# Performance work log

Hardware: AMD Instinct MI355X
Metric: run time of the kernel (lower is better)

The kernel has to match this reference:

```python
import jax, jax.numpy as jnp
import numpy as np

B, NX, NY = 4, 2048, 2048
DIM = 1024        # model dimension
IN_DIM = 1024    # input_dimension
OUT_DIM = 1024   # output_dimension
NUM_HEADS = 16
HEAD_DIM = DIM // NUM_HEADS
SCALE = HEAD_DIM ** -0.5


def setup_inputs() -> dict:
    key = jax.random.key(0)
    kx, ky, kq, kkv, ko = jax.random.split(key, 5)
    x = jax.random.normal(kx, (B, NX, IN_DIM), dtype=jnp.float32)
    y = jax.random.normal(ky, (B, NY, IN_DIM), dtype=jnp.float32)
    # Linear weights (stored as [in, out]; bias=False in the original)
    Wq = jax.random.normal(kq, (IN_DIM, DIM), dtype=jnp.float32) * (IN_DIM ** -0.5)
    Wkv = jax.random.normal(kkv, (IN_DIM, 2 * DIM), dtype=jnp.float32) * (IN_DIM ** -0.5)
    Wo = jax.random.normal(ko, (DIM, OUT_DIM), dtype=jnp.float32) * (DIM ** -0.5)
    return {"x": x, "y": y, "Wq": Wq, "Wkv": Wkv, "Wo": Wo}


def reference(x, y, Wq, Wkv, Wo):
    Bv, Nx, _ = x.shape
    Ny = y.shape[1]
    # projections
    q = (x @ Wq).reshape(Bv, Nx, NUM_HEADS, HEAD_DIM)          # [B,Nx,H,hd]
    kv = (y @ Wkv).reshape(Bv, Ny, 2, NUM_HEADS, HEAD_DIM)     # [B,Ny,2,H,hd]
    k, v = kv[:, :, 0], kv[:, :, 1]                            # [B,Ny,H,hd]
    # attention scores [B,H,Nx,Ny]
    attn = jax.nn.softmax(jnp.einsum('bqhd,bkhd->bhqk', q, k) * SCALE, axis=-1)
    # weighted values -> [B,Nx,H,hd] -> [B,Nx,DIM]
    r = jnp.einsum('bhqk,bkhd->bqhd', attn, v).reshape(Bv, Nx, DIM)
    return r @ Wo
```

## Files before the change

kernel.cpp:

```cpp
#include <hip/hip_runtime.h>
#include <cstdint>

typedef unsigned short u16;
typedef __bf16 bf16x8 __attribute__((ext_vector_type(8)));
typedef short  s16x4  __attribute__((ext_vector_type(4)));
typedef float  f32x4  __attribute__((ext_vector_type(4)));

#define BB 4
#define NX 2048
#define NY 2048
#define DIM 1024
#define IN_DIM 1024
#define NH 16
#define HD 64
#define SL (0.125f * 1.4426950408889634f)

#if __has_builtin(__builtin_amdgcn_exp2f)
#define EXP2(x) __builtin_amdgcn_exp2f(x)
#else
#define EXP2(x) exp2f(x)
#endif

#if __has_builtin(__builtin_amdgcn_cvt_pk_bf16_f32)
#define HAS_PKBF16 1
#else
#define HAS_PKBF16 0
#endif

__device__ __forceinline__ u16 f2bf(float f) {
    unsigned int u = __builtin_bit_cast(unsigned int, f);
    unsigned int r = (u + 0x7FFFu + ((u >> 16) & 1u)) >> 16;
    return (u16)r;
}

__device__ __forceinline__ unsigned int pk2(float a, float b) {
#if HAS_PKBF16
    auto t = __builtin_amdgcn_cvt_pk_bf16_f32(a, b);
    return __builtin_bit_cast(unsigned int, t);
#else
    return (unsigned int)f2bf(a) | ((unsigned int)f2bf(b) << 16);
#endif
}

__device__ __forceinline__ unsigned int pk2t(float a, float b) {
    return __builtin_amdgcn_perm(__builtin_bit_cast(unsigned int, b),
                                 __builtin_bit_cast(unsigned int, a),
                                 0x07060302u);
}

__device__ __forceinline__ float truncbf(float f) {
    return __builtin_bit_cast(float,
        __builtin_bit_cast(unsigned int, f) & 0xFFFF0000u);
}

__device__ __forceinline__ void gl_lds16(const u16* g, u16* l) {
    __builtin_amdgcn_global_load_lds(
        (const __attribute__((address_space(1))) unsigned int*)g,
        (__attribute__((address_space(3))) unsigned int*)l, 16, 0, 0);
}

__global__ __launch_bounds__(256) void prep(const float* __restrict__ x,
                                            const float* __restrict__ y,
                                            const float* __restrict__ Wq,
                                            const float* __restrict__ Wkv,
                                            const float* __restrict__ Wo,
                                            u16* __restrict__ xb,
                                            u16* __restrict__ yb,
                                            u16* __restrict__ WqT,
                                            u16* __restrict__ WkvT,
                                            u16* __restrict__ WoT) {
    const int bx = blockIdx.x;
    if (bx < 16384) {
        const float* in = (bx < 8192) ? x : y;
        u16* out = (bx < 8192) ? xb : yb;
        int i = (bx & 8191) * 256 + threadIdx.x;
        float4 v = ((const float4*)in)[i];
        ushort4 o;
        o.x = f2bf(v.x); o.y = f2bf(v.y); o.z = f2bf(v.z); o.w = f2bf(v.w);
        ((ushort4*)out)[i] = o;
    } else {
        __shared__ u16 t[32 * 33];
        int id = bx - 16384;
        int nx = id & 127;
        const int k0 = (id >> 7) * 32;
        const float* W; u16* Wt; int N;
        if (nx < 32)      { W = Wq;  Wt = WqT;  N = 1024; }
        else if (nx < 96) { W = Wkv; Wt = WkvT; N = 2048; nx -= 32; }
        else              { W = Wo;  Wt = WoT;  N = 1024; nx -= 96; }
        const int K = 1024;
        const int tid = threadIdx.x;
        const int col = tid & 31, rw = tid >> 5;
        const int n0 = nx * 32;
#pragma unroll
        for (int i = 0; i < 4; i++) {
            int k = rw + i * 8;
            float v = W[(size_t)(k0 + k) * N + n0 + col];
            t[col * 33 + k] = f2bf(v);
        }
        __syncthreads();
#pragma unroll
        for (int i = 0; i < 4; i++) {
            int n = rw + i * 8;
            Wt[(size_t)(n0 + n) * K + k0 + col] = t[n * 33 + col];
        }
    }
}

__global__ __launch_bounds__(256) void transpose_v(const u16* __restrict__ kv,
                                                   u16* __restrict__ vT) {
    __shared__ u16 t[64 * 72];
    const int tid = threadIdx.x;
    const int bh = blockIdx.x;
    const int b = bh >> 4, h = bh & 15;
    const int y0 = blockIdx.y * 64;
    {
        int y = tid >> 2, dc = tid & 3;
        const u16* src = &kv[((size_t)(b * NY + y0 + y)) * (2 * DIM) + DIM + h * HD + dc * 16];
        uint4 v0 = *(const uint4*)src;
        uint4 v1 = *(const uint4*)(src + 8);
        u16 tmp[16];
        *(uint4*)&tmp[0] = v0;
        *(uint4*)&tmp[8] = v1;
#pragma unroll
        for (int i = 0; i < 16; i++) t[(dc * 16 + i) * 72 + y] = tmp[i];
    }
    __syncthreads();
    {
        int d = tid >> 2, yc = tid & 3;
        uint4 v0 = *(const uint4*)&t[d * 72 + yc * 16];
        uint4 v1 = *(const uint4*)&t[d * 72 + yc * 16 + 8];
        u16* dst = &vT[((size_t)bh * HD + d) * NY + y0 + yc * 16];
        *(uint4*)dst = v0;
        *(uint4*)(dst + 8) = v1;
    }
}

template <bool BF16OUT, int TN>
__device__ __forceinline__ void gemm_core(u16* As, u16* Bs,
                                          const u16* __restrict__ A,
                                          const u16* __restrict__ Bt,
                                          void* __restrict__ Cv,
                                          int N, int K, float oscale,
                                          int m0, int n0) {
    constexpr int NJ = TN / 32;
    u16* Cb = (u16*)Cv;
    float* Cf = (float*)Cv;
    const int tid = threadIdx.x;
    const int wave = tid >> 6, lane = tid & 63;
    const int ml = lane & 15, qd = lane >> 4;
    const int mlo = ml & 7;
    const int wm = (wave >> 1) * 64, wn = (wave & 1) * (TN / 2);

    f32x4 acc[4][NJ];
#pragma unroll
    for (int i = 0; i < 4; i++)
#pragma unroll
        for (int j = 0; j < NJ; j++)
#pragma unroll
            for (int e = 0; e < 4; e++) acc[i][j][e] = 0.0f;

    const int r0 = tid >> 3;
    const int swz = (tid & 7) ^ (r0 & 7);
    const u16* Ap = A + (size_t)(m0 + r0) * K + swz * 8;
    const u16* Bp = Bt + (size_t)(n0 + r0) * K + swz * 8;

    for (int k0 = 0; k0 < K; k0 += 64) {
        __syncthreads();
#pragma unroll
        for (int i = 0; i < 4; i++)
            gl_lds16(Ap + (size_t)(i * 32) * K + k0, &As[(i * 256 + wave * 64) * 8]);
#pragma unroll
        for (int i = 0; i < TN / 32; i++)
            gl_lds16(Bp + (size_t)(i * 32) * K + k0, &Bs[(i * 256 + wave * 64) * 8]);
        __syncthreads();

#pragma unroll
        for (int s = 0; s < 2; s++) {
            bf16x8 af[4], bfr[NJ];
#pragma unroll
            for (int i = 0; i < 4; i++)
                af[i] = *(const bf16x8*)&As[(wm + i * 16 + ml) * 64 + (((s * 4 + qd) ^ mlo) * 8)];
#pragma unroll
            for (int j = 0; j < NJ; j++)
                bfr[j] = *(const bf16x8*)&Bs[(wn + j * 16 + ml) * 64 + (((s * 4 + qd) ^ mlo) * 8)];
#pragma unroll
            for (int i = 0; i < 4; i++)
#pragma unroll
                for (int j = 0; j < NJ; j++)
                    acc[i][j] = __builtin_amdgcn_mfma_f32_16x16x32_bf16(af[i], bfr[j], acc[i][j], 0, 0, 0);
        }
    }

#pragma unroll
    for (int i = 0; i < 4; i++)
#pragma unroll
        for (int j = 0; j < NJ; j++)
#pragma unroll
            for (int r = 0; r < 4; r++) {
                int row = m0 + wm + i * 16 + qd * 4 + r;
                int col = n0 + wn + j * 16 + ml;
                if (BF16OUT) Cb[(size_t)row * N + col] = f2bf(acc[i][j][r] * oscale);
                else         Cf[(size_t)row * N + col] = acc[i][j][r];
            }
}

__global__ __launch_bounds__(256) void gemm_proj(const u16* __restrict__ xb,
                                                 const u16* __restrict__ yb,
                                                 const u16* __restrict__ WqT,
                                                 const u16* __restrict__ WkvT,
                                                 u16* __restrict__ qb,
                                                 u16* __restrict__ kvb) {
    __shared__ u16 As[128 * 64];
    __shared__ u16 Bs[128 * 64];
    const bool isq = blockIdx.x < 8;
    const u16* A  = isq ? xb : yb;
    const u16* Bt = isq ? WqT : WkvT;
    u16* C        = isq ? qb : kvb;
    const int N   = isq ? 1024 : 2048;
    const int n0  = (isq ? blockIdx.x : blockIdx.x - 8) * 128;
    const float oscale = isq ? SL : 1.0f;
    gemm_core<true, 128>(As, Bs, A, Bt, C, N, 1024, oscale, blockIdx.y * 128, n0);
}

__global__ __launch_bounds__(256, 4) void gemm_o(const u16* __restrict__ A,
                                                 const u16* __restrict__ Bt,
                                                 float* __restrict__ C) {
    __shared__ u16 As[128 * 64];
    __shared__ u16 Bs[64 * 64];
    gemm_core<false, 64>(As, Bs, A, Bt, C, 1024, 1024, 1.0f, blockIdx.y * 128, blockIdx.x * 64);
}

__global__ __launch_bounds__(256, 4) void flash_attn(const u16* __restrict__ qg,
                                                     const u16* __restrict__ kvg,
                                                     const u16* __restrict__ vTg,
                                                     u16* __restrict__ rg) {
    __shared__ u16 Kt[2][64 * 64];
    __shared__ u16 Vt[2][64 * 64];
    const int tid = threadIdx.x, wave = tid >> 6, lane = tid & 63;
    const int ml = lane & 15, qd = lane >> 4;
    const int xt = blockIdx.x, bh = blockIdx.y;
    const int b = bh >> 4, h = bh & 15;
    const int mlo = ml & 7;

    bf16x8 aq[2][2];
    {
        size_t qbase = ((size_t)(b * NX + xt * 128 + wave * 32)) * DIM + h * HD;
#pragma unroll
        for (int mt = 0; mt < 2; mt++)
#pragma unroll
            for (int s = 0; s < 2; s++)
                aq[mt][s] = *(const bf16x8*)&qg[qbase + (size_t)(mt * 16 + ml) * DIM + s * 32 + qd * 8];
    }

    int ka[2];
#pragma unroll
    for (int s = 0; s < 2; s++) ka[s] = ml * 128 + (((s * 4 + qd) ^ mlo) << 4);
    int va[2][2];
#pragma unroll
    for (int t2 = 0; t2 < 2; t2++)
#pragma unroll
        for (int hh = 0; hh < 2; hh++)
            va[t2][hh] = ml * 128 + ((((t2 * 4 + 2 * hh + (qd >> 1)) ^ mlo) * 8 + (qd & 1) * 4) << 1);
    const char* Kb = (const char*)&Kt[0][0];
    const char* Vb = (const char*)&Vt[0][0];

    const int rloc = lane >> 3;
    const int swz = (lane & 7) ^ rloc;
    const u16* ksrc[2];
    const u16* vsrc[2];
#pragma unroll
    for (int e = 0; e < 2; e++) {
        int row = (wave * 2 + e) * 8 + rloc;
        ksrc[e] = kvg + ((size_t)(b * NY + row)) * (2 * DIM) + h * HD + swz * 8;
        vsrc[e] = vTg + ((size_t)(bh * HD + row)) * NY + swz * 8;
    }
    const size_t KSTRIDE = (size_t)64 * (2 * DIM);
    const size_t VSTRIDE = 64;

    f32x4 o[2][4];
    f32x4 li4[2];
#pragma unroll
    for (int mt = 0; mt < 2; mt++) {
#pragma unroll
        for (int e = 0; e < 4; e++) li4[mt][e] = 0.0f;
#pragma unroll
        for (int dt = 0; dt < 4; dt++)
#pragma unroll
            for (int e = 0; e < 4; e++) o[mt][dt][e] = 0.0f;
    }
    const f32x4 fz = {0.0f, 0.0f, 0.0f, 0.0f};

#pragma unroll
    for (int e = 0; e < 2; e++) { gl_lds16(ksrc[e], &Kt[0][(wave * 2 + e) * 512]); ksrc[e] += KSTRIDE; }
#pragma unroll
    for (int e = 0; e < 2; e++) { gl_lds16(vsrc[e], &Vt[0][(wave * 2 + e) * 512]); vsrc[e] += VSTRIDE; }

    for (int it = 0; it < NY / 64; it += 2) {
#pragma unroll
        for (int half = 0; half < 2; ++half) {
            __syncthreads();
            if (it + half + 1 < NY / 64) {
#pragma unroll
                for (int e = 0; e < 2; e++) { gl_lds16(ksrc[e], &Kt[half ^ 1][(wave * 2 + e) * 512]); ksrc[e] += KSTRIDE; }
#pragma unroll
                for (int e = 0; e < 2; e++) { gl_lds16(vsrc[e], &Vt[half ^ 1][(wave * 2 + e) * 512]); vsrc[e] += VSTRIDE; }
            }

            f32x4 sc[2][4];
#pragma unroll
            for (int t = 0; t < 4; t++) {
                bf16x8 kf0 = *(const bf16x8*)(Kb + (half * 8192 + t * 2048) + ka[0]);
                bf16x8 kf1 = *(const bf16x8*)(Kb + (half * 8192 + t * 2048) + ka[1]);
                sc[0][t] = __builtin_amdgcn_mfma_f32_16x16x32_bf16(kf0, aq[0][0], fz, 0, 0, 0);
                sc[1][t] = __builtin_amdgcn_mfma_f32_16x16x32_bf16(kf0, aq[1][0], fz, 0, 0, 0);
                sc[0][t] = __builtin_amdgcn_mfma_f32_16x16x32_bf16(kf1, aq[0][1], sc[0][t], 0, 0, 0);
                sc[1][t] = __builtin_amdgcn_mfma_f32_16x16x32_bf16(kf1, aq[1][1], sc[1][t], 0, 0, 0);
            }

            uint4 pb[2][2];
#pragma unroll
            for (int mt = 0; mt < 2; mt++) {
#pragma unroll
                for (int t = 0; t < 4; t++)
#pragma unroll
                    for (int r = 0; r < 4; r++) sc[mt][t][r] = EXP2(sc[mt][t][r]);
#if HAS_PKBF16
                li4[mt] += (sc[mt][0] + sc[mt][1]) + (sc[mt][2] + sc[mt][3]);
#pragma unroll
                for (int t2 = 0; t2 < 2; t2++) {
                    pb[mt][t2].x = pk2(sc[mt][2 * t2][0], sc[mt][2 * t2][1]);
                    pb[mt][t2].y = pk2(sc[mt][2 * t2][2], sc[mt][2 * t2][3]);
                    pb[mt][t2].z = pk2(sc[mt][2 * t2 + 1][0], sc[mt][2 * t2 + 1][1]);
                    pb[mt][t2].w = pk2(sc[mt][2 * t2 + 1][2], sc[mt][2 * t2 + 1][3]);
                }
#else
#pragma unroll
                for (int t = 0; t < 4; t++)
#pragma unroll
                    for (int r = 0; r < 4; r++) sc[mt][t][r] = truncbf(sc[mt][t][r]);
                li4[mt] += (sc[mt][0] + sc[mt][1]) + (sc[mt][2] + sc[mt][3]);
#pragma unroll
                for (int t2 = 0; t2 < 2; t2++) {
                    pb[mt][t2].x = pk2t(sc[mt][2 * t2][0], sc[mt][2 * t2][1]);
                    pb[mt][t2].y = pk2t(sc[mt][2 * t2][2], sc[mt][2 * t2][3]);
                    pb[mt][t2].z = pk2t(sc[mt][2 * t2 + 1][0], sc[mt][2 * t2 + 1][1]);
                    pb[mt][t2].w = pk2t(sc[mt][2 * t2 + 1][2], sc[mt][2 * t2 + 1][3]);
                }
#endif
            }

#pragma unroll
            for (int t2 = 0; t2 < 2; t2++) {
                bf16x8 p0 = __builtin_bit_cast(bf16x8, pb[0][t2]);
                bf16x8 p1 = __builtin_bit_cast(bf16x8, pb[1][t2]);
#pragma unroll
                for (int dt = 0; dt < 4; dt++) {
                    union { struct { s16x4 lo, hi; } p; bf16x8 v; } u;
                    u.p.lo = *(const s16x4*)(Vb + (half * 8192 + dt * 2048) + va[t2][0]);
                    u.p.hi = *(const s16x4*)(Vb + (half * 8192 + dt * 2048) + va[t2][1]);
                    o[0][dt] = __builtin_amdgcn_mfma_f32_16x16x32_bf16(u.v, p0, o[0][dt], 0, 0, 0);
                    o[1][dt] = __builtin_amdgcn_mfma_f32_16x16x32_bf16(u.v, p1, o[1][dt], 0, 0, 0);
                }
            }
        }
    }

#pragma unroll
    for (int mt = 0; mt < 2; mt++) {
        float l = (li4[mt][0] + li4[mt][1]) + (li4[mt][2] + li4[mt][3]);
        l += __shfl_xor(l, 16);
        l += __shfl_xor(l, 32);
        float inv = 1.0f / l;
        size_t row = (size_t)(b * NX + xt * 128 + wave * 32 + mt * 16 + ml);
#pragma unroll
        for (int dt = 0; dt < 4; dt++) {
            uint2 val;
            val.x = pk2(o[mt][dt][0] * inv, o[mt][dt][1] * inv);
            val.y = pk2(o[mt][dt][2] * inv, o[mt][dt][3] * inv);
            *(uint2*)&rg[row * DIM + h * HD + dt * 16 + qd * 4] = val;
        }
    }
}

extern "C" void kernel_launch(void* const* d_in, const int* in_sizes, int n_in,
                              void* d_out, int out_size, void* d_ws, size_t ws_size,
                              hipStream_t stream) {
    const float* x   = (const float*)d_in[0];
    const float* y   = (const float*)d_in[1];
    const float* Wq  = (const float*)d_in[2];
    const float* Wkv = (const float*)d_in[3];
    const float* Wo  = (const float*)d_in[4];

    char* ws = (char*)d_ws;
    u16* xb   = (u16*)(ws + 0);
    u16* yb   = (u16*)(ws + 16777216);
    u16* WqT  = (u16*)(ws + 33554432);
    u16* WkvT = (u16*)(ws + 35651584);
    u16* WoT  = (u16*)(ws + 39845888);
    u16* qb   = (u16*)(ws + 41943040);
    u16* kvb  = (u16*)(ws + 58720256);
    u16* vTb  = (u16*)(ws + 92274688);
    u16* rb   = (u16*)(ws + 109051904);

    prep<<<20480, 256, 0, stream>>>(x, y, Wq, Wkv, Wo, xb, yb, WqT, WkvT, WoT);

    gemm_proj<<<dim3(24, 64), 256, 0, stream>>>(xb, yb, WqT, WkvT, qb, kvb);

    transpose_v<<<dim3(64, 32), 256, 0, stream>>>(kvb, vTb);

    flash_attn<<<dim3(16, 64), 256, 0, stream>>>(qb, kvb, vTb, rb);

    gemm_o<<<dim3(16, 64), 256, 0, stream>>>(rb, WoT, (float*)d_out);
}
```

Measured before the change: 305.4 us.

## Fuse V transpose into projection GEMM epilogue and simplify V fragment loads

The projection GEMM now writes K to a compact [B,NY,1024] buffer and writes V directly in a transposed, permuted per-head layout from its epilogue, so the separate transpose_v kernel and its extra read and write of V go away. The permuted V layout lets flash attention read each V fragment with one 16-byte LDS load reusing the K swizzle offsets instead of two 8-byte loads. The cost is a more complex, less coalesced scattered epilogue store in the GEMM, and correctness depends on the permutation matching the P fragment ordering.

```diff
diff --git a/kernel.cpp b/kernel.cpp
--- a/kernel.cpp
+++ b/kernel.cpp
@@ -3,7 +3,6 @@
 
 typedef unsigned short u16;
 typedef __bf16 bf16x8 __attribute__((ext_vector_type(8)));
-typedef short  s16x4  __attribute__((ext_vector_type(4)));
 typedef float  f32x4  __attribute__((ext_vector_type(4)));
 
 #define BB 4
@@ -106,52 +105,19 @@
     }
 }
 
-__global__ __launch_bounds__(256) void transpose_v(const u16* __restrict__ kv,
-                                                   u16* __restrict__ vT) {
-    __shared__ u16 t[64 * 72];
-    const int tid = threadIdx.x;
-    const int bh = blockIdx.x;
-    const int b = bh >> 4, h = bh & 15;
-    const int y0 = blockIdx.y * 64;
-    {
-        int y = tid >> 2, dc = tid & 3;
-        const u16* src = &kv[((size_t)(b * NY + y0 + y)) * (2 * DIM) + DIM + h * HD + dc * 16];
-        uint4 v0 = *(const uint4*)src;
-        uint4 v1 = *(const uint4*)(src + 8);
-        u16 tmp[16];
-        *(uint4*)&tmp[0] = v0;
-        *(uint4*)&tmp[8] = v1;
-#pragma unroll
-        for (int i = 0; i < 16; i++) t[(dc * 16 + i) * 72 + y] = tmp[i];
-    }
-    __syncthreads();
-    {
-        int d = tid >> 2, yc = tid & 3;
-        uint4 v0 = *(const uint4*)&t[d * 72 + yc * 16];
-        uint4 v1 = *(const uint4*)&t[d * 72 + yc * 16 + 8];
-        u16* dst = &vT[((size_t)bh * HD + d) * NY + y0 + yc * 16];
-        *(uint4*)dst = v0;
-        *(uint4*)(dst + 8) = v1;
-    }
-}
-
-template <bool BF16OUT, int TN>
-__device__ __forceinline__ void gemm_core(u16* As, u16* Bs,
-                                          const u16* __restrict__ A,
-                                          const u16* __restrict__ Bt,
-                                          void* __restrict__ Cv,
-                                          int N, int K, float oscale,
-                                          int m0, int n0) {
+template <int TN>
+__device__ __forceinline__ void gemm_accum(u16* As, u16* Bs,
+                                           const u16* __restrict__ A,
+                                           const u16* __restrict__ Bt,
+                                           int K, int m0, int n0,
+                                           f32x4 (&acc)[4][TN / 32]) {
     constexpr int NJ = TN / 32;
-    u16* Cb = (u16*)Cv;
-    float* Cf = (float*)Cv;
     const int tid = threadIdx.x;
     const int wave = tid >> 6, lane = tid & 63;
     const int ml = lane & 15, qd = lane >> 4;
     const int mlo = ml & 7;
     const int wm = (wave >> 1) * 64, wn = (wave & 1) * (TN / 2);
 
-    f32x4 acc[4][NJ];
 #pragma unroll
     for (int i = 0; i < 4; i++)
 #pragma unroll
@@ -190,18 +156,6 @@
                     acc[i][j] = __builtin_amdgcn_mfma_f32_16x16x32_bf16(af[i], bfr[j], acc[i][j], 0, 0, 0);
         }
     }
-
-#pragma unroll
-    for (int i = 0; i < 4; i++)
-#pragma unroll
-        for (int j = 0; j < NJ; j++)
-#pragma unroll
-            for (int r = 0; r < 4; r++) {
-                int row = m0 + wm + i * 16 + qd * 4 + r;
-                int col = n0 + wn + j * 16 + ml;
-                if (BF16OUT) Cb[(size_t)row * N + col] = f2bf(acc[i][j][r] * oscale);
-                else         Cf[(size_t)row * N + col] = acc[i][j][r];
-            }
 }
 
 __global__ __launch_bounds__(256) void gemm_proj(const u16* __restrict__ xb,
@@ -209,17 +163,56 @@
                                                  const u16* __restrict__ WqT,
                                                  const u16* __restrict__ WkvT,
                                                  u16* __restrict__ qb,
-                                                 u16* __restrict__ kvb) {
+                                                 u16* __restrict__ kb,
+                                                 u16* __restrict__ vT) {
     __shared__ u16 As[128 * 64];
     __shared__ u16 Bs[128 * 64];
+    const int tid = threadIdx.x;
+    const int wave = tid >> 6, lane = tid & 63;
+    const int ml = lane & 15, qd = lane >> 4;
+    const int m0 = blockIdx.y * 128;
     const bool isq = blockIdx.x < 8;
-    const u16* A  = isq ? xb : yb;
-    const u16* Bt = isq ? WqT : WkvT;
-    u16* C        = isq ? qb : kvb;
-    const int N   = isq ? 1024 : 2048;
-    const int n0  = (isq ? blockIdx.x : blockIdx.x - 8) * 128;
-    const float oscale = isq ? SL : 1.0f;
-    gemm_core<true, 128>(As, Bs, A, Bt, C, N, 1024, oscale, blockIdx.y * 128, n0);
+    const int n0 = (isq ? blockIdx.x : blockIdx.x - 8) * 128;
+
+    f32x4 acc[4][4];
+    if (isq) gemm_accum<128>(As, Bs, xb, WqT, 1024, m0, n0, acc);
+    else     gemm_accum<128>(As, Bs, yb, WkvT, 1024, m0, n0, acc);
+
+    const int wm = (wave >> 1) * 64, wn = (wave & 1) * 64;
+
+    if (isq || n0 < 1024) {
+        u16* C = isq ? qb : kb;
+        const float oscale = isq ? SL : 1.0f;
+#pragma unroll
+        for (int i = 0; i < 4; i++)
+#pragma unroll
+            for (int j = 0; j < 4; j++)
+#pragma unroll
+                for (int r = 0; r < 4; r++) {
+                    int row = m0 + wm + i * 16 + qd * 4 + r;
+                    int col = n0 + wn + j * 16 + ml;
+                    C[(size_t)row * 1024 + col] = f2bf(acc[i][j][r] * oscale);
+                }
+    } else {
+        const int b = m0 >> 11;
+        const int yy0 = m0 & 2047;
+        const int dg0 = n0 - 1024 + wn;
+#pragma unroll
+        for (int i = 0; i < 4; i++) {
+            const int yy32 = ((wm + i * 16) >> 5) << 5;
+            const int yoff = yy0 + yy32 + 8 * qd + 4 * (i & 1);
+#pragma unroll
+            for (int j = 0; j < 4; j++) {
+                int dg = dg0 + j * 16 + ml;
+                int h = dg >> 6, d = dg & 63;
+                size_t base = ((size_t)((b * NH + h) * HD + d)) * NY + yoff;
+                uint2 val;
+                val.x = pk2(acc[i][j][0], acc[i][j][1]);
+                val.y = pk2(acc[i][j][2], acc[i][j][3]);
+                *(uint2*)&vT[base] = val;
+            }
+        }
+    }
 }
 
 __global__ __launch_bounds__(256, 4) void gemm_o(const u16* __restrict__ A,
@@ -227,11 +220,29 @@
                                                  float* __restrict__ C) {
     __shared__ u16 As[128 * 64];
     __shared__ u16 Bs[64 * 64];
-    gemm_core<false, 64>(As, Bs, A, Bt, C, 1024, 1024, 1.0f, blockIdx.y * 128, blockIdx.x * 64);
+    const int tid = threadIdx.x;
+    const int wave = tid >> 6, lane = tid & 63;
+    const int ml = lane & 15, qd = lane >> 4;
+    const int m0 = blockIdx.y * 128, n0 = blockIdx.x * 64;
+
+    f32x4 acc[4][2];
+    gemm_accum<64>(As, Bs, A, Bt, 1024, m0, n0, acc);
+
+    const int wm = (wave >> 1) * 64, wn = (wave & 1) * 32;
+#pragma unroll
+    for (int i = 0; i < 4; i++)
+#pragma unroll
+        for (int j = 0; j < 2; j++)
+#pragma unroll
+            for (int r = 0; r < 4; r++) {
+                int row = m0 + wm + i * 16 + qd * 4 + r;
+                int col = n0 + wn + j * 16 + ml;
+                C[(size_t)row * 1024 + col] = acc[i][j][r];
+            }
 }
 
 __global__ __launch_bounds__(256, 4) void flash_attn(const u16* __restrict__ qg,
-                                                     const u16* __restrict__ kvg,
+                                                     const u16* __restrict__ kg,
                                                      const u16* __restrict__ vTg,
                                                      u16* __restrict__ rg) {
     __shared__ u16 Kt[2][64 * 64];
@@ -255,12 +266,6 @@
     int ka[2];
 #pragma unroll
     for (int s = 0; s < 2; s++) ka[s] = ml * 128 + (((s * 4 + qd) ^ mlo) << 4);
-    int va[2][2];
-#pragma unroll
-    for (int t2 = 0; t2 < 2; t2++)
-#pragma unroll
-        for (int hh = 0; hh < 2; hh++)
-            va[t2][hh] = ml * 128 + ((((t2 * 4 + 2 * hh + (qd >> 1)) ^ mlo) * 8 + (qd & 1) * 4) << 1);
     const char* Kb = (const char*)&Kt[0][0];
     const char* Vb = (const char*)&Vt[0][0];
 
@@ -271,10 +276,10 @@
 #pragma unroll
     for (int e = 0; e < 2; e++) {
         int row = (wave * 2 + e) * 8 + rloc;
-        ksrc[e] = kvg + ((size_t)(b * NY + row)) * (2 * DIM) + h * HD + swz * 8;
+        ksrc[e] = kg + ((size_t)(b * NY + row)) * 1024 + h * HD + swz * 8;
         vsrc[e] = vTg + ((size_t)(bh * HD + row)) * NY + swz * 8;
     }
-    const size_t KSTRIDE = (size_t)64 * (2 * DIM);
+    const size_t KSTRIDE = (size_t)64 * 1024;
     const size_t VSTRIDE = 64;
 
     f32x4 o[2][4];
@@ -355,11 +360,9 @@
                 bf16x8 p1 = __builtin_bit_cast(bf16x8, pb[1][t2]);
 #pragma unroll
                 for (int dt = 0; dt < 4; dt++) {
-                    union { struct { s16x4 lo, hi; } p; bf16x8 v; } u;
-                    u.p.lo = *(const s16x4*)(Vb + (half * 8192 + dt * 2048) + va[t2][0]);
-                    u.p.hi = *(const s16x4*)(Vb + (half * 8192 + dt * 2048) + va[t2][1]);
-                    o[0][dt] = __builtin_amdgcn_mfma_f32_16x16x32_bf16(u.v, p0, o[0][dt], 0, 0, 0);
-                    o[1][dt] = __builtin_amdgcn_mfma_f32_16x16x32_bf16(u.v, p1, o[1][dt], 0, 0, 0);
+                    bf16x8 vv = *(const bf16x8*)(Vb + (half * 8192 + dt * 2048) + ka[t2]);
+                    o[0][dt] = __builtin_amdgcn_mfma_f32_16x16x32_bf16(vv, p0, o[0][dt], 0, 0, 0);
+                    o[1][dt] = __builtin_amdgcn_mfma_f32_16x16x32_bf16(vv, p1, o[1][dt], 0, 0, 0);
                 }
             }
         }
@@ -398,17 +401,15 @@
     u16* WkvT = (u16*)(ws + 35651584);
     u16* WoT  = (u16*)(ws + 39845888);
     u16* qb   = (u16*)(ws + 41943040);
-    u16* kvb  = (u16*)(ws + 58720256);
+    u16* kb   = (u16*)(ws + 58720256);
     u16* vTb  = (u16*)(ws + 92274688);
     u16* rb   = (u16*)(ws + 109051904);
 
     prep<<<20480, 256, 0, stream>>>(x, y, Wq, Wkv, Wo, xb, yb, WqT, WkvT, WoT);
 
-    gemm_proj<<<dim3(24, 64), 256, 0, stream>>>(xb, yb, WqT, WkvT, qb, kvb);
-
-    transpose_v<<<dim3(64, 32), 256, 0, stream>>>(kvb, vTb);
-
-    flash_attn<<<dim3(16, 64), 256, 0, stream>>>(qb, kvb, vTb, rb);
+    gemm_proj<<<dim3(24, 64), 256, 0, stream>>>(xb, yb, WqT, WkvT, qb, kb, vTb);
+
+    flash_attn<<<dim3(16, 64), 256, 0, stream>>>(qb, kb, vTb, rb);
 
     gemm_o<<<dim3(16, 64), 256, 0, stream>>>(rb, WoT, (float*)d_out);
 }
```

After: 299.8 us. No clear change (-1.9%).
